# Performance work log

Measured on AMD Instinct MI355X. Metric: run time of the kernel, lower is better.

Reference implementation:

```python
import jax, jax.numpy as jnp
import numpy as np

ALPHA = 0.9  # EMAFusion temporal_fusion_alpha


def setup_inputs() -> dict:
    key = jax.random.key(0)
    y_seq = jax.random.normal(key, (4, 4096, 2048), dtype=jnp.float32)
    return {"y_seq": y_seq}


def reference(y_seq):
    # EMA recurrence: h_t = (1-alpha)*y_t + alpha*h_{t-1}, h_{-1}=0.
    # Original torch code detaches h_prev each step (backward-only effect),
    # mirrored here with stop_gradient on the carry.
    B, S, D = y_seq.shape
    h0 = jnp.zeros((B, D), dtype=y_seq.dtype)

    def step(h_prev, y_t):
        h_prev = jax.lax.stop_gradient(h_prev)
        h_t = (1.0 - ALPHA) * y_t + ALPHA * h_prev
        return h_t, h_t

    # scan over time axis: move S to leading dim
    _, out = jax.lax.scan(step, h0, jnp.swapaxes(y_seq, 0, 1))  # (S, B, D)
    return jnp.swapaxes(out, 0, 1)  # (B, S, D)
```

## Files before the change

### kernel.cpp

```cpp
#include <hip/hip_runtime.h>


typedef float v4 __attribute__((ext_vector_type(4)));

constexpr int B  = 4;
constexpr int S  = 4096;
constexpr int D  = 2048;
constexpr int D4 = D / 4;
constexpr int L  = 32;
constexpr int W  = 64;

__global__ __launch_bounds__(256, 4) void ema_kernel(const v4* __restrict__ y,
                                                     v4* __restrict__ out) {
    const int d4 = blockIdx.x * blockDim.x + threadIdx.x;
    const int c  = blockIdx.y;
    const int b  = blockIdx.z;

    const long long base = (long long)b * S * D4 + d4;
    const int sm = c * L;

    v4 h = (v4)(0.0f);
    const v4* __restrict__ p;

    v4 a0, a1, a2, a3, a4, a5, a6, a7;
    v4 b0, b1, b2, b3, b4, b5, b6, b7;

#define LOADA() do {               \
        a0 = p[0 * D4];            \
        a1 = p[1 * D4];            \
        a2 = p[2 * D4];            \
        a3 = p[3 * D4];            \
        a4 = p[4 * D4];            \
        a5 = p[5 * D4];            \
        a6 = p[6 * D4];            \
        a7 = p[7 * D4];            \
        p += 8 * D4;               \
    } while (0)

#define LOADB() do {               \
        b0 = p[0 * D4];            \
        b1 = p[1 * D4];            \
        b2 = p[2 * D4];            \
        b3 = p[3 * D4];            \
        b4 = p[4 * D4];            \
        b5 = p[5 * D4];            \
        b6 = p[6 * D4];            \
        b7 = p[7 * D4];            \
        p += 8 * D4;               \
    } while (0)

#define EMA(x) (h = 0.9f * h + 0.1f * (x))
#define EMAA() do { EMA(a0); EMA(a1); EMA(a2); EMA(a3); \
                    EMA(a4); EMA(a5); EMA(a6); EMA(a7); } while (0)
#define EMAB() do { EMA(b0); EMA(b1); EMA(b2); EMA(b3); \
                    EMA(b4); EMA(b5); EMA(b6); EMA(b7); } while (0)

    const int nw = (sm < W) ? sm : W;
    p = y + base + (long long)(sm - nw) * D4;

    if (nw) {
        LOADA();
        LOADB();
        #pragma unroll 1
        for (int g = 0; g < (nw / 8 - 2) / 2; ++g) {
            EMAA(); LOADA();
            EMAB(); LOADB();
        }
        EMAA();
        EMAB();
    }

    v4* __restrict__ q = out + base + (long long)sm * D4;

    LOADA();
    LOADB();

    EMA(a0); __builtin_nontemporal_store(h, q + 0 * D4);
    EMA(a1); __builtin_nontemporal_store(h, q + 1 * D4);
    EMA(a2); __builtin_nontemporal_store(h, q + 2 * D4);
    EMA(a3); __builtin_nontemporal_store(h, q + 3 * D4);
    EMA(a4); __builtin_nontemporal_store(h, q + 4 * D4);
    EMA(a5); __builtin_nontemporal_store(h, q + 5 * D4);
    EMA(a6); __builtin_nontemporal_store(h, q + 6 * D4);
    EMA(a7); __builtin_nontemporal_store(h, q + 7 * D4);
    LOADA();

    EMA(b0); __builtin_nontemporal_store(h, q +  8 * D4);
    EMA(b1); __builtin_nontemporal_store(h, q +  9 * D4);
    EMA(b2); __builtin_nontemporal_store(h, q + 10 * D4);
    EMA(b3); __builtin_nontemporal_store(h, q + 11 * D4);
    EMA(b4); __builtin_nontemporal_store(h, q + 12 * D4);
    EMA(b5); __builtin_nontemporal_store(h, q + 13 * D4);
    EMA(b6); __builtin_nontemporal_store(h, q + 14 * D4);
    EMA(b7); __builtin_nontemporal_store(h, q + 15 * D4);
    LOADB();

    EMA(a0); __builtin_nontemporal_store(h, q + 16 * D4);
    EMA(a1); __builtin_nontemporal_store(h, q + 17 * D4);
    EMA(a2); __builtin_nontemporal_store(h, q + 18 * D4);
    EMA(a3); __builtin_nontemporal_store(h, q + 19 * D4);
    EMA(a4); __builtin_nontemporal_store(h, q + 20 * D4);
    EMA(a5); __builtin_nontemporal_store(h, q + 21 * D4);
    EMA(a6); __builtin_nontemporal_store(h, q + 22 * D4);
    EMA(a7); __builtin_nontemporal_store(h, q + 23 * D4);

    EMA(b0); __builtin_nontemporal_store(h, q + 24 * D4);
    EMA(b1); __builtin_nontemporal_store(h, q + 25 * D4);
    EMA(b2); __builtin_nontemporal_store(h, q + 26 * D4);
    EMA(b3); __builtin_nontemporal_store(h, q + 27 * D4);
    EMA(b4); __builtin_nontemporal_store(h, q + 28 * D4);
    EMA(b5); __builtin_nontemporal_store(h, q + 29 * D4);
    EMA(b6); __builtin_nontemporal_store(h, q + 30 * D4);
    EMA(b7); __builtin_nontemporal_store(h, q + 31 * D4);

#undef EMAB
#undef EMAA
#undef EMA
#undef LOADB
#undef LOADA
}

extern "C" void kernel_launch(void* const* d_in, const int* in_sizes, int n_in,
                              void* d_out, int out_size, void* d_ws, size_t ws_size,
                              hipStream_t stream) {
    const v4* y = (const v4*)d_in[0];
    v4* out = (v4*)d_out;

    dim3 block(256, 1, 1);
    dim3 grid(D4 / 256, S / L, B);
    ema_kernel<<<grid, block, 0, stream>>>(y, out);
}
```

Measured before the change: 255.2 us.

## Lengthen per-block time chunk to cut warmup re-reads, add sched barriers

```diff
diff --git a/kernel.cpp b/kernel.cpp
--- a/kernel.cpp
+++ b/kernel.cpp
@@ -7,10 +7,12 @@
 constexpr int S  = 4096;
 constexpr int D  = 2048;
 constexpr int D4 = D / 4;
-constexpr int L  = 32;
+constexpr int L  = 128;
 constexpr int W  = 64;
 
-__global__ __launch_bounds__(256, 4) void ema_kernel(const v4* __restrict__ y,
+#define SB() __builtin_amdgcn_sched_barrier(0)
+
+__global__ __launch_bounds__(256, 1) void ema_kernel(const v4* __restrict__ y,
                                                      v4* __restrict__ out) {
     const int d4 = blockIdx.x * blockDim.x + threadIdx.x;
     const int c  = blockIdx.y;
@@ -20,7 +22,7 @@
     const int sm = c * L;
 
     v4 h = (v4)(0.0f);
-    const v4* __restrict__ p;
+    const v4* p;
 
     v4 a0, a1, a2, a3, a4, a5, a6, a7;
     v4 b0, b1, b2, b3, b4, b5, b6, b7;
@@ -55,64 +57,59 @@
 #define EMAB() do { EMA(b0); EMA(b1); EMA(b2); EMA(b3); \
                     EMA(b4); EMA(b5); EMA(b6); EMA(b7); } while (0)
 
-    const int nw = (sm < W) ? sm : W;
-    p = y + base + (long long)(sm - nw) * D4;
-
-    if (nw) {
-        LOADA();
-        LOADB();
+    if (c != 0) {
+        p = y + base + (long long)(sm - W) * D4;
+        LOADA(); SB();
+        LOADB(); SB();
         #pragma unroll 1
-        for (int g = 0; g < (nw / 8 - 2) / 2; ++g) {
-            EMAA(); LOADA();
-            EMAB(); LOADB();
+        for (int g = 0; g < W / 16 - 1; ++g) {
+            EMAA(); LOADA(); SB();
+            EMAB(); LOADB(); SB();
         }
         EMAA();
-        EMAB();
+        EMAB(); SB();
+    } else {
+        p = y + base;
     }
 
-    v4* __restrict__ q = out + base + (long long)sm * D4;
+    v4* q = out + base + (long long)sm * D4;
 
-    LOADA();
-    LOADB();
+#define STA() do {                                              \
+        EMA(a0); __builtin_nontemporal_store(h, q + 0 * D4);    \
+        EMA(a1); __builtin_nontemporal_store(h, q + 1 * D4);    \
+        EMA(a2); __builtin_nontemporal_store(h, q + 2 * D4);    \
+        EMA(a3); __builtin_nontemporal_store(h, q + 3 * D4);    \
+        EMA(a4); __builtin_nontemporal_store(h, q + 4 * D4);    \
+        EMA(a5); __builtin_nontemporal_store(h, q + 5 * D4);    \
+        EMA(a6); __builtin_nontemporal_store(h, q + 6 * D4);    \
+        EMA(a7); __builtin_nontemporal_store(h, q + 7 * D4);    \
+    } while (0)
 
-    EMA(a0); __builtin_nontemporal_store(h, q + 0 * D4);
-    EMA(a1); __builtin_nontemporal_store(h, q + 1 * D4);
-    EMA(a2); __builtin_nontemporal_store(h, q + 2 * D4);
-    EMA(a3); __builtin_nontemporal_store(h, q + 3 * D4);
-    EMA(a4); __builtin_nontemporal_store(h, q + 4 * D4);
-    EMA(a5); __builtin_nontemporal_store(h, q + 5 * D4);
-    EMA(a6); __builtin_nontemporal_store(h, q + 6 * D4);
-    EMA(a7); __builtin_nontemporal_store(h, q + 7 * D4);
-    LOADA();
+#define STB() do {                                              \
+        EMA(b0); __builtin_nontemporal_store(h, q +  8 * D4);   \
+        EMA(b1); __builtin_nontemporal_store(h, q +  9 * D4);   \
+        EMA(b2); __builtin_nontemporal_store(h, q + 10 * D4);   \
+        EMA(b3); __builtin_nontemporal_store(h, q + 11 * D4);   \
+        EMA(b4); __builtin_nontemporal_store(h, q + 12 * D4);   \
+        EMA(b5); __builtin_nontemporal_store(h, q + 13 * D4);   \
+        EMA(b6); __builtin_nontemporal_store(h, q + 14 * D4);   \
+        EMA(b7); __builtin_nontemporal_store(h, q + 15 * D4);   \
+    } while (0)
 
-    EMA(b0); __builtin_nontemporal_store(h, q +  8 * D4);
-    EMA(b1); __builtin_nontemporal_store(h, q +  9 * D4);
-    EMA(b2); __builtin_nontemporal_store(h, q + 10 * D4);
-    EMA(b3); __builtin_nontemporal_store(h, q + 11 * D4);
-    EMA(b4); __builtin_nontemporal_store(h, q + 12 * D4);
-    EMA(b5); __builtin_nontemporal_store(h, q + 13 * D4);
-    EMA(b6); __builtin_nontemporal_store(h, q + 14 * D4);
-    EMA(b7); __builtin_nontemporal_store(h, q + 15 * D4);
-    LOADB();
+    LOADA(); SB();
+    LOADB(); SB();
 
-    EMA(a0); __builtin_nontemporal_store(h, q + 16 * D4);
-    EMA(a1); __builtin_nontemporal_store(h, q + 17 * D4);
-    EMA(a2); __builtin_nontemporal_store(h, q + 18 * D4);
-    EMA(a3); __builtin_nontemporal_store(h, q + 19 * D4);
-    EMA(a4); __builtin_nontemporal_store(h, q + 20 * D4);
-    EMA(a5); __builtin_nontemporal_store(h, q + 21 * D4);
-    EMA(a6); __builtin_nontemporal_store(h, q + 22 * D4);
-    EMA(a7); __builtin_nontemporal_store(h, q + 23 * D4);
+    #pragma unroll 1
+    for (int g = 0; g < L / 16 - 1; ++g) {
+        STA(); LOADA(); SB();
+        STB(); LOADB(); SB();
+        q += 16 * D4;
+    }
+    STA();
+    STB();
 
-    EMA(b0); __builtin_nontemporal_store(h, q + 24 * D4);
-    EMA(b1); __builtin_nontemporal_store(h, q + 25 * D4);
-    EMA(b2); __builtin_nontemporal_store(h, q + 26 * D4);
-    EMA(b3); __builtin_nontemporal_store(h, q + 27 * D4);
-    EMA(b4); __builtin_nontemporal_store(h, q + 28 * D4);
-    EMA(b5); __builtin_nontemporal_store(h, q + 29 * D4);
-    EMA(b6); __builtin_nontemporal_store(h, q + 30 * D4);
-    EMA(b7); __builtin_nontemporal_store(h, q + 31 * D4);
-
+#undef STB
+#undef STA
 #undef EMAB
 #undef EMAA
 #undef EMA
```

Result: faster. 237.0 us (-7.1%).
